# Optimization experiments

Measured on AMD Instinct MI355X. Metric: run time of the kernel, lower is better.

## Reference

```python
import jax, jax.numpy as jnp
import numpy as np

B, S, D, H, Dh, F = 1, 2048, 2048, 24, 128, 8192  # batch, seq, dim, heads, dim_head, ff hidden
SCALE = Dh ** -0.5


def _layernorm(x, g, b, eps=1e-5):
    mu = jnp.mean(x, axis=-1, keepdims=True)
    var = jnp.var(x, axis=-1, keepdims=True)
    return (x - mu) * jax.lax.rsqrt(var + eps) * g + b


def _rmsnorm(x, g, eps=1e-5):
    ms = jnp.mean(jnp.square(x), axis=-1, keepdims=True)
    return x * jax.lax.rsqrt(ms + eps) * g


def setup_inputs() -> dict:
    key = jax.random.key(0)
    ks = jax.random.split(key, 8)
    w = lambda k, sh: (jax.random.normal(k, sh, jnp.float32) * (1.0 / np.sqrt(sh[0]))).astype(jnp.float32)
    return {
        "x": jax.random.normal(ks[0], (B, S, D), jnp.float32),
        "ln_g": jnp.ones((D,), jnp.float32),
        "ln_b": jnp.zeros((D,), jnp.float32),
        "attn_g": jnp.ones((D,), jnp.float32),  # RingAttention prenorm (RMSNorm) gamma
        "Wq": w(ks[1], (D, H * Dh)),
        "Wk": w(ks[2], (D, H * Dh)),
        "Wv": w(ks[3], (D, H * Dh)),
        "Wo": w(ks[4], (H * Dh, D)),
        "W1": w(ks[5], (D, F)),
        "b1": jnp.zeros((F,), jnp.float32),
        "W2": w(ks[6], (F, D)),
        "b2": jnp.zeros((D,), jnp.float32),
    }


def reference(x, ln_g, ln_b, attn_g, Wq, Wk, Wv, Wo, W1, b1, W2, b2):
    # outer block LayerNorm
    x = _layernorm(x, ln_g, ln_b)

    # --- causal multi-head attention (math-equivalent to ring attention) ---
    h = _rmsnorm(x, attn_g)  # attention's internal prenorm
    q = (h @ Wq).reshape(B, S, H, Dh)
    k = (h @ Wk).reshape(B, S, H, Dh)
    v = (h @ Wv).reshape(B, S, H, Dh)
    scores = jnp.einsum("bqhd,bkhd->bhqk", q, k) * SCALE  # [B,H,S,S]
    causal = jnp.tril(jnp.ones((S, S), bool))
    scores = jnp.where(causal, scores, jnp.finfo(scores.dtype).min)
    attn = jax.nn.softmax(scores, axis=-1)
    o = jnp.einsum("bhqk,bkhd->bqhd", attn, v).reshape(B, S, H * Dh)
    x = o @ Wo + x  # residual

    # --- feedforward + residual ---
    x = jax.nn.gelu(x @ W1 + b1) @ W2 + b2 + x
    return x
```

## Files before the change

kernel.cpp:

```cpp
#include <hip/hip_runtime.h>
#include <hip/hip_bf16.h>

#define Sq 2048
#define Dm 2048
#define HDim 3072
#define QKVDim 9216
#define NH 24
#define DH 128
#define FF 8192
#define ATT_SCALE 0.08838834764831845f

using bf16 = __hip_bfloat16;
typedef __attribute__((ext_vector_type(8))) short bf16x8;
typedef __attribute__((ext_vector_type(4))) float f32x4;
typedef unsigned int u32;
typedef unsigned long long u64;
typedef __attribute__((ext_vector_type(4))) u32 u32x4;

__device__ __forceinline__ void gload_lds16(const void* g, void* l) {
    __builtin_amdgcn_global_load_lds(
        (const __attribute__((address_space(1))) void*)g,
        (__attribute__((address_space(3))) void*)l, 16, 0, 0);
}

__global__ __launch_bounds__(256) void ln_rms_kernel(
    const float* __restrict__ x, const float* __restrict__ g, const float* __restrict__ b,
    const float* __restrict__ ag, float* __restrict__ xnf, bf16* __restrict__ h)
{
    __shared__ float redA[4], redB[4], redC[4];
    int row = blockIdx.x;
    int t = threadIdx.x;
    int lane = t & 63, wid = t >> 6;
    const float* xr = x + (size_t)row * Dm;

    float v[8];
    float sum = 0.f, ssq = 0.f;
#pragma unroll
    for (int i = 0; i < 8; i++) {
        float f = xr[t + 256 * i];
        v[i] = f; sum += f; ssq += f * f;
    }
#pragma unroll
    for (int off = 32; off > 0; off >>= 1) {
        sum += __shfl_down(sum, off);
        ssq += __shfl_down(ssq, off);
    }
    if (lane == 0) { redA[wid] = sum; redB[wid] = ssq; }
    __syncthreads();
    sum = redA[0] + redA[1] + redA[2] + redA[3];
    ssq = redB[0] + redB[1] + redB[2] + redB[3];
    float mu = sum * (1.f / Dm);
    float var = ssq * (1.f / Dm) - mu * mu;
    float rstd = rsqrtf(var + 1e-5f);

    float xn[8];
    float s2 = 0.f;
#pragma unroll
    for (int i = 0; i < 8; i++) {
        int col = t + 256 * i;
        float xv = (v[i] - mu) * rstd * g[col] + b[col];
        xn[i] = xv;
        xnf[(size_t)row * Dm + col] = xv;
        s2 += xv * xv;
    }
#pragma unroll
    for (int off = 32; off > 0; off >>= 1) s2 += __shfl_down(s2, off);
    if (lane == 0) redC[wid] = s2;
    __syncthreads();
    s2 = redC[0] + redC[1] + redC[2] + redC[3];
    float rms = rsqrtf(s2 * (1.f / Dm) + 1e-5f);
#pragma unroll
    for (int i = 0; i < 8; i++) {
        int col = t + 256 * i;
        h[(size_t)row * Dm + col] = __float2bfloat16(xn[i] * rms * ag[col]);
    }
}

__global__ __launch_bounds__(256) void transpose_cvt_kernel(
    const float* __restrict__ W, bf16* __restrict__ Wt, int K, int N)
{
    __shared__ float tile[64][65];
    int n0 = blockIdx.x * 64, k0 = blockIdx.y * 64;
    int t = threadIdx.x;
    int lr = t >> 4, lc = (t & 15) * 4;
#pragma unroll
    for (int i = 0; i < 4; i++) {
        int r = lr + i * 16;
        f32x4 v = *reinterpret_cast<const f32x4*>(W + (size_t)(k0 + r) * N + n0 + lc);
        *reinterpret_cast<f32x4*>(&tile[r][lc]) = v;
    }
    __syncthreads();
    int nr = t >> 3, kc = (t & 7) * 8;
#pragma unroll
    for (int i = 0; i < 2; i++) {
        int n = nr + i * 32;
        bf16 o8[8];
#pragma unroll
        for (int j = 0; j < 8; j++) o8[j] = __float2bfloat16(tile[kc + j][n]);
        *reinterpret_cast<u32x4*>(Wt + (size_t)(n0 + n) * K + k0 + kc) =
            *reinterpret_cast<const u32x4*>(o8);
    }
}

__global__ __launch_bounds__(256) void transpose_cvt3_kernel(
    const float* __restrict__ Wa, const float* __restrict__ Wb, const float* __restrict__ Wc,
    bf16* __restrict__ Wt, int K, int N)
{
    __shared__ float tile[64][65];
    const float* W = blockIdx.z == 0 ? Wa : (blockIdx.z == 1 ? Wb : Wc);
    bf16* dst = Wt + (size_t)blockIdx.z * N * K;
    int n0 = blockIdx.x * 64, k0 = blockIdx.y * 64;
    int t = threadIdx.x;
    int lr = t >> 4, lc = (t & 15) * 4;
#pragma unroll
    for (int i = 0; i < 4; i++) {
        int r = lr + i * 16;
        f32x4 v = *reinterpret_cast<const f32x4*>(W + (size_t)(k0 + r) * N + n0 + lc);
        *reinterpret_cast<f32x4*>(&tile[r][lc]) = v;
    }
    __syncthreads();
    int nr = t >> 3, kc = (t & 7) * 8;
#pragma unroll
    for (int i = 0; i < 2; i++) {
        int n = nr + i * 32;
        bf16 o8[8];
#pragma unroll
        for (int j = 0; j < 8; j++) o8[j] = __float2bfloat16(tile[kc + j][n]);
        *reinterpret_cast<u32x4*>(dst + (size_t)(n0 + n) * K + k0 + kc) =
            *reinterpret_cast<const u32x4*>(o8);
    }
}

__global__ __launch_bounds__(256) void cvt_prefill_kernel(
    const float* __restrict__ xnf, const float* __restrict__ bias,
    bf16* __restrict__ hb, float* __restrict__ o, int N)
{
    int i = (blockIdx.x * 256 + threadIdx.x) * 8;
    int col = i % N;
    f32x4 a = *reinterpret_cast<const f32x4*>(xnf + i);
    f32x4 b = *reinterpret_cast<const f32x4*>(xnf + i + 4);
    bf16 r[8];
#pragma unroll
    for (int j = 0; j < 4; j++) { r[j] = __float2bfloat16(a[j]); r[4 + j] = __float2bfloat16(b[j]); }
    *reinterpret_cast<u32x4*>(hb + i) = *reinterpret_cast<const u32x4*>(r);
    f32x4 b0 = *reinterpret_cast<const f32x4*>(bias + col);
    f32x4 b1v = *reinterpret_cast<const f32x4*>(bias + col + 4);
    f32x4 o0 = {a[0] + b0[0], a[1] + b0[1], a[2] + b0[2], a[3] + b0[3]};
    f32x4 o1 = {b[0] + b1v[0], b[1] + b1v[1], b[2] + b1v[2], b[3] + b1v[3]};
    *reinterpret_cast<f32x4*>(o + i) = o0;
    *reinterpret_cast<f32x4*>(o + i + 4) = o1;
}

template <int EPI>
__global__ __launch_bounds__(256, 4) void gemm_kernel(
    const bf16* __restrict__ A, const bf16* __restrict__ Bt,
    int M, int N, int K, int Ksplit,
    bf16* Cb, float* Cf, const float* __restrict__ bias)
{
    __shared__ __align__(16) bf16 As[128 * 64];
    __shared__ __align__(16) bf16 Bs[128 * 64];
    int m0 = blockIdx.y * 128, n0 = blockIdx.x * 128;
    int kbeg = blockIdx.z * Ksplit, kend = kbeg + Ksplit;
    int tid = threadIdx.x;
    int lane = tid & 63, w = tid >> 6;
    int wr = w >> 1, wc = w & 1;
    int l15 = lane & 15, lhi = lane >> 4;

    int srow = lane >> 3;
    int scol = ((lane & 7) ^ (lane >> 3)) * 8;

    const f32x4 zero4 = {0.f, 0.f, 0.f, 0.f};
    f32x4 acc[4][4];
#pragma unroll
    for (int m = 0; m < 4; m++)
#pragma unroll
        for (int n = 0; n < 4; n++) acc[m][n] = zero4;

    for (int k0 = kbeg; k0 < kend; k0 += 64) {
        __syncthreads();
#pragma unroll
        for (int c = 0; c < 4; c++) {
            int row = w * 32 + c * 8 + srow;
            gload_lds16(A + (size_t)(m0 + row) * K + k0 + scol,
                        (char*)As + w * 4096 + c * 1024);
            gload_lds16(Bt + (size_t)(n0 + row) * K + k0 + scol,
                        (char*)Bs + w * 4096 + c * 1024);
        }
        __syncthreads();
#pragma unroll
        for (int ks = 0; ks < 2; ks++) {
            bf16x8 af[4], bfr[4];
#pragma unroll
            for (int m = 0; m < 4; m++) {
                int r = wr * 64 + m * 16 + l15;
                af[m] = *reinterpret_cast<const bf16x8*>(
                    &As[r * 64 + (((ks << 2) + lhi) ^ (r & 7)) * 8]);
            }
#pragma unroll
            for (int n = 0; n < 4; n++) {
                int r = wc * 64 + n * 16 + l15;
                bfr[n] = *reinterpret_cast<const bf16x8*>(
                    &Bs[r * 64 + (((ks << 2) + lhi) ^ (r & 7)) * 8]);
            }
#pragma unroll
            for (int m = 0; m < 4; m++)
#pragma unroll
                for (int n = 0; n < 4; n++)
                    acc[m][n] = __builtin_amdgcn_mfma_f32_16x16x32_bf16(af[m], bfr[n], acc[m][n], 0, 0, 0);
        }
    }

#pragma unroll
    for (int m = 0; m < 4; m++) {
        int row = m0 + wr * 64 + m * 16 + lhi * 4;
#pragma unroll
        for (int n = 0; n < 4; n++) {
            int col = n0 + wc * 64 + n * 16 + l15;
#pragma unroll
            for (int j = 0; j < 4; j++) {
                float vv = acc[m][n][j];
                size_t idx = (size_t)(row + j) * N + col;
                if (EPI == 0) {
                    Cb[idx] = __float2bfloat16(vv);
                } else if (EPI == 2) {
                    float o = vv + bias[col];
                    float u = 1.5957691216057308f * (o + 0.044715f * o * o * o);
                    Cb[idx] = __float2bfloat16(o / (1.0f + __expf(-u)));
                } else {
                    atomicAdd(&Cf[idx], vv);
                }
            }
        }
    }
}

__global__ __launch_bounds__(512) void attn_kernel(
    const bf16* __restrict__ qkv, bf16* __restrict__ o)
{
    __shared__ __align__(16) bf16 KsF[2][64 * 128];
    __shared__ __align__(16) bf16 VtF[128 * 72];
    __shared__ __align__(16) bf16 Pl[8][16][76];
    int rank = blockIdx.x;
    int qb = (Sq / 128 - 1) - rank / NH;
    int head = rank % NH;
    const bf16* q = qkv + head * DH;
    const bf16* k = qkv + HDim + head * DH;
    const bf16* v = qkv + 2 * HDim + head * DH;
    int tid = threadIdx.x, lane = tid & 63, w = tid >> 6;
    int l15 = lane & 15, lhi = lane >> 4;
    int qrow0 = qb * 128 + w * 16;

    bf16x8 aq[4];
    const bf16* qbase = q + (size_t)(qrow0 + l15) * QKVDim;
#pragma unroll
    for (int kk = 0; kk < 4; kk++)
        aq[kk] = *reinterpret_cast<const bf16x8*>(qbase + kk * 32 + lhi * 8);

    bf16x8 vones;
#pragma unroll
    for (int j = 0; j < 8; j++) vones[j] = (short)0x3F80;

    int vkv = lhi * 2 + (w & 1) + (w >> 1) * 8;
    int vd0 = l15 * 8;
    int vxr = l15 & 7;
    const bf16* vbase = v + (size_t)vkv * QKVDim + vd0;

    const f32x4 zero4 = {0.f, 0.f, 0.f, 0.f};
    f32x4 acc_o[8];
#pragma unroll
    for (int db = 0; db < 8; db++) acc_o[db] = zero4;
    f32x4 acc_l = zero4;
    float mrow[4];
#pragma unroll
    for (int r = 0; r < 4; r++) mrow[r] = -1e30f;

    int nt = 2 * qb + 2;

    {
#pragma unroll
        for (int c = 0; c < 2; c++) {
            int row = w * 8 + c * 4 + lhi;
            int cb = l15 ^ (row & 7);
            gload_lds16(k + (size_t)row * QKVDim + cb * 8,
                        (char*)&KsF[0][0] + w * 2048 + c * 1024);
        }
#pragma unroll
        for (int i = 0; i < 2; i++) {
            int kv = vkv + i * 32;
            bf16x8 vv = *reinterpret_cast<const bf16x8*>(vbase + (size_t)(i * 32) * QKVDim);
            int vb = kv >> 3, kr = kv & 7;
#pragma unroll
            for (int j = 0; j < 8; j++)
                VtF[(vd0 + j) * 72 + ((vb ^ vxr) << 3) + kr] = ((const bf16*)&vv)[j];
        }
        __syncthreads();
    }

    for (int kb = 0; kb < nt; kb++) {
        int kv0 = kb * 64;
        int p = kb & 1;
        bf16x8 vreg[2];
        bool pref = (kb + 1 < nt);
        if (pref) {
            int nv0 = kv0 + 64;
#pragma unroll
            for (int c = 0; c < 2; c++) {
                int row = w * 8 + c * 4 + lhi;
                int cb = l15 ^ (row & 7);
                gload_lds16(k + (size_t)(nv0 + row) * QKVDim + cb * 8,
                            (char*)&KsF[p ^ 1][0] + w * 2048 + c * 1024);
            }
#pragma unroll
            for (int i = 0; i < 2; i++)
                vreg[i] = *reinterpret_cast<const bf16x8*>(
                    vbase + (size_t)(nv0 + i * 32) * QKVDim);
        }

        bool active = (kv0 <= qrow0 + 15);
        if (active) {
            f32x4 sacc[4];
            __builtin_amdgcn_s_setprio(1);
#pragma unroll
            for (int nb = 0; nb < 4; nb++) {
                sacc[nb] = zero4;
                int krow = nb * 16 + l15;
#pragma unroll
                for (int kk = 0; kk < 4; kk++) {
                    const char* kp = (const char*)&KsF[p][0] + krow * 256 +
                                     ((kk * 64 + lhi * 16) ^ ((krow & 7) << 4));
                    bf16x8 bk = *reinterpret_cast<const bf16x8*>(kp);
                    sacc[nb] = __builtin_amdgcn_mfma_f32_16x16x32_bf16(aq[kk], bk, sacc[nb], 0, 0, 0);
                }
            }
            __builtin_amdgcn_s_setprio(0);

            bool msk = (kv0 + 63 > qrow0);
            float sv[4][4];
            float pm[4];
#pragma unroll
            for (int r = 0; r < 4; r++) pm[r] = -1e30f;
#pragma unroll
            for (int nb = 0; nb < 4; nb++) {
                int kvc = kv0 + nb * 16 + l15;
#pragma unroll
                for (int r = 0; r < 4; r++) {
                    int qr = qrow0 + lhi * 4 + r;
                    float s = sacc[nb][r] * ATT_SCALE;
                    if (msk && kvc > qr) s = -1e30f;
                    sv[nb][r] = s;
                    pm[r] = fmaxf(pm[r], s);
                }
            }
#pragma unroll
            for (int off = 1; off < 16; off <<= 1)
#pragma unroll
                for (int r = 0; r < 4; r++)
                    pm[r] = fmaxf(pm[r], __shfl_xor(pm[r], off));

            float nm[4];
            bool need = false;
#pragma unroll
            for (int r = 0; r < 4; r++) {
                nm[r] = fmaxf(mrow[r], pm[r]);
                need = need || (pm[r] > mrow[r] + 8.f);
            }
            if (__any(need)) {
#pragma unroll
                for (int r = 0; r < 4; r++) {
                    float sc = __expf(mrow[r] - nm[r]);
                    mrow[r] = nm[r];
                    acc_l[r] *= sc;
#pragma unroll
                    for (int db = 0; db < 8; db++) acc_o[db][r] *= sc;
                }
            }

#pragma unroll
            for (int nb = 0; nb < 4; nb++)
#pragma unroll
                for (int r = 0; r < 4; r++)
                    sv[nb][r] = __expf(sv[nb][r] - mrow[r]);

#pragma unroll
            for (int nb = 0; nb < 4; nb++)
#pragma unroll
                for (int r = 0; r < 4; r++)
                    Pl[w][lhi * 4 + r][nb * 16 + l15] = __float2bfloat16(sv[nb][r]);

            __builtin_amdgcn_s_setprio(1);
#pragma unroll
            for (int ks = 0; ks < 2; ks++) {
                bf16x8 ap = *reinterpret_cast<const bf16x8*>(&Pl[w][l15][ks * 32 + lhi * 8]);
                acc_l = __builtin_amdgcn_mfma_f32_16x16x32_bf16(ap, vones, acc_l, 0, 0, 0);
#pragma unroll
                for (int db = 0; db < 8; db++) {
                    int dv = db * 16 + l15;
                    int blk = (ks * 4 + lhi) ^ ((dv >> 3) & 7);
                    bf16x8 bv = *reinterpret_cast<const bf16x8*>(&VtF[dv * 72 + blk * 8]);
                    acc_o[db] = __builtin_amdgcn_mfma_f32_16x16x32_bf16(ap, bv, acc_o[db], 0, 0, 0);
                }
            }
            __builtin_amdgcn_s_setprio(0);
        }

        __syncthreads();
        if (pref) {
#pragma unroll
            for (int i = 0; i < 2; i++) {
                int kv = vkv + i * 32;
                int vb = kv >> 3, kr = kv & 7;
#pragma unroll
                for (int j = 0; j < 8; j++)
                    VtF[(vd0 + j) * 72 + ((vb ^ vxr) << 3) + kr] = ((const bf16*)&vreg[i])[j];
            }
        }
        __syncthreads();
    }

#pragma unroll
    for (int db = 0; db < 8; db++)
#pragma unroll
        for (int r = 0; r < 4; r++) {
            int qr = qrow0 + lhi * 4 + r;
            float val = acc_o[db][r] / acc_l[r];
            o[(size_t)qr * HDim + head * DH + db * 16 + l15] = __float2bfloat16(val);
        }
}

extern "C" void kernel_launch(void* const* d_in, const int* in_sizes, int n_in,
                              void* d_out, int out_size, void* d_ws, size_t ws_size,
                              hipStream_t stream)
{
    const float* x     = (const float*)d_in[0];
    const float* ln_g  = (const float*)d_in[1];
    const float* ln_b  = (const float*)d_in[2];
    const float* attng = (const float*)d_in[3];
    const float* Wq    = (const float*)d_in[4];
    const float* Wk    = (const float*)d_in[5];
    const float* Wv    = (const float*)d_in[6];
    const float* Wo    = (const float*)d_in[7];
    const float* W1    = (const float*)d_in[8];
    const float* b1    = (const float*)d_in[9];
    const float* W2    = (const float*)d_in[10];
    const float* b2    = (const float*)d_in[11];
    float* out = (float*)d_out;
    char* ws = (char*)d_ws;

    bf16*  wbuf = (bf16*)(ws + 0);
    float* xnf  = (float*)(ws + 39845888);
    bf16*  hbuf = (bf16*)(ws + 56623104);
    bf16*  qkv  = (bf16*)(ws + 65011712);
    bf16*  ob_  = (bf16*)(ws + 102760448);
    bf16*  gb_  = qkv;

    ln_rms_kernel<<<Sq, 256, 0, stream>>>(x, ln_g, ln_b, attng, xnf, hbuf);

    transpose_cvt3_kernel<<<dim3(HDim / 64, Dm / 64, 3), 256, 0, stream>>>(
        Wq, Wk, Wv, wbuf, Dm, HDim);
    gemm_kernel<0><<<dim3(QKVDim / 128, Sq / 128, 1), 256, 0, stream>>>(
        hbuf, wbuf, Sq, QKVDim, Dm, Dm, qkv, nullptr, nullptr);

    attn_kernel<<<dim3(NH * Sq / 128), 512, 0, stream>>>(qkv, ob_);

    transpose_cvt_kernel<<<dim3(Dm / 64, HDim / 64), 256, 0, stream>>>(Wo, wbuf, HDim, Dm);
    gemm_kernel<4><<<dim3(Dm / 128, Sq / 128, 2), 256, 0, stream>>>(
        ob_, wbuf, Sq, Dm, HDim, HDim / 2, nullptr, xnf, nullptr);
    cvt_prefill_kernel<<<(Sq * Dm) / (256 * 8), 256, 0, stream>>>(xnf, b2, hbuf, out, Dm);

    transpose_cvt_kernel<<<dim3(FF / 64, Dm / 64), 256, 0, stream>>>(W1, wbuf, Dm, FF);
    gemm_kernel<2><<<dim3(FF / 128, Sq / 128, 1), 256, 0, stream>>>(
        hbuf, wbuf, Sq, FF, Dm, Dm, gb_, nullptr, b1);

    transpose_cvt_kernel<<<dim3(Dm / 64, FF / 64), 256, 0, stream>>>(W2, wbuf, FF, Dm);
    gemm_kernel<4><<<dim3(Dm / 128, Sq / 128, 2), 256, 0, stream>>>(
        gb_, wbuf, Sq, Dm, FF, FF / 2, nullptr, out, nullptr);
}
```

Measured before the change: 449.3 us.

## Merge weight transposes into LN and attention launches; use exp2 softmax

The Wq/Wk/Wv transpose-convert now runs as extra blocks of the LayerNorm/RMSNorm kernel, and the Wo transpose as extra blocks of the attention kernel, each selected by block index and sharing LDS through a union. This removes two kernel launches and lets the independent transpose work fill idle compute units while the other blocks run. The attention softmax now folds log2(e) into the score scale and uses exp2f, with the rescale threshold adjusted to match. The cost is larger LDS and register footprints in the merged kernels, which may lower occupancy for the main work.

```diff
diff --git a/kernel.cpp b/kernel.cpp
--- a/kernel.cpp
+++ b/kernel.cpp
@@ -9,6 +9,7 @@
 #define DH 128
 #define FF 8192
 #define ATT_SCALE 0.08838834764831845f
+#define ATT_SCALE2 0.12752534331809017f
 
 using bf16 = __hip_bfloat16;
 typedef __attribute__((ext_vector_type(8))) short bf16x8;
@@ -23,13 +24,49 @@
         (__attribute__((address_space(3))) void*)l, 16, 0, 0);
 }
 
-__global__ __launch_bounds__(256) void ln_rms_kernel(
+__global__ __launch_bounds__(256) void ln_qkvt_kernel(
     const float* __restrict__ x, const float* __restrict__ g, const float* __restrict__ b,
-    const float* __restrict__ ag, float* __restrict__ xnf, bf16* __restrict__ h)
+    const float* __restrict__ ag, float* __restrict__ xnf, bf16* __restrict__ h,
+    const float* __restrict__ Wq, const float* __restrict__ Wk, const float* __restrict__ Wv,
+    bf16* __restrict__ Wt)
 {
-    __shared__ float redA[4], redB[4], redC[4];
-    int row = blockIdx.x;
+    union SmemU {
+        float red[12];
+        float tile[64][65];
+    };
+    __shared__ SmemU sm;
+    int bid = blockIdx.x;
     int t = threadIdx.x;
+
+    if (bid >= Sq) {
+        int tb = bid - Sq;
+        int z = tb / 1536, rr = tb % 1536;
+        int bx = rr % 48, by = rr / 48;
+        const float* W = z == 0 ? Wq : (z == 1 ? Wk : Wv);
+        bf16* dst = Wt + (size_t)z * HDim * Dm;
+        int n0 = bx * 64, k0 = by * 64;
+        int lr = t >> 4, lc = (t & 15) * 4;
+#pragma unroll
+        for (int i = 0; i < 4; i++) {
+            int r = lr + i * 16;
+            f32x4 v = *reinterpret_cast<const f32x4*>(W + (size_t)(k0 + r) * HDim + n0 + lc);
+            *reinterpret_cast<f32x4*>(&sm.tile[r][lc]) = v;
+        }
+        __syncthreads();
+        int nr = t >> 3, kc = (t & 7) * 8;
+#pragma unroll
+        for (int i = 0; i < 2; i++) {
+            int n = nr + i * 32;
+            bf16 o8[8];
+#pragma unroll
+            for (int j = 0; j < 8; j++) o8[j] = __float2bfloat16(sm.tile[kc + j][n]);
+            *reinterpret_cast<u32x4*>(dst + (size_t)(n0 + n) * Dm + k0 + kc) =
+                *reinterpret_cast<const u32x4*>(o8);
+        }
+        return;
+    }
+
+    int row = bid;
     int lane = t & 63, wid = t >> 6;
     const float* xr = x + (size_t)row * Dm;
 
@@ -45,10 +82,10 @@
         sum += __shfl_down(sum, off);
         ssq += __shfl_down(ssq, off);
     }
-    if (lane == 0) { redA[wid] = sum; redB[wid] = ssq; }
+    if (lane == 0) { sm.red[wid] = sum; sm.red[4 + wid] = ssq; }
     __syncthreads();
-    sum = redA[0] + redA[1] + redA[2] + redA[3];
-    ssq = redB[0] + redB[1] + redB[2] + redB[3];
+    sum = sm.red[0] + sm.red[1] + sm.red[2] + sm.red[3];
+    ssq = sm.red[4] + sm.red[5] + sm.red[6] + sm.red[7];
     float mu = sum * (1.f / Dm);
     float var = ssq * (1.f / Dm) - mu * mu;
     float rstd = rsqrtf(var + 1e-5f);
@@ -65,9 +102,9 @@
     }
 #pragma unroll
     for (int off = 32; off > 0; off >>= 1) s2 += __shfl_down(s2, off);
-    if (lane == 0) redC[wid] = s2;
+    if (lane == 0) sm.red[8 + wid] = s2;
     __syncthreads();
-    s2 = redC[0] + redC[1] + redC[2] + redC[3];
+    s2 = sm.red[8] + sm.red[9] + sm.red[10] + sm.red[11];
     float rms = rsqrtf(s2 * (1.f / Dm) + 1e-5f);
 #pragma unroll
     for (int i = 0; i < 8; i++) {
@@ -98,35 +135,6 @@
 #pragma unroll
         for (int j = 0; j < 8; j++) o8[j] = __float2bfloat16(tile[kc + j][n]);
         *reinterpret_cast<u32x4*>(Wt + (size_t)(n0 + n) * K + k0 + kc) =
-            *reinterpret_cast<const u32x4*>(o8);
-    }
-}
-
-__global__ __launch_bounds__(256) void transpose_cvt3_kernel(
-    const float* __restrict__ Wa, const float* __restrict__ Wb, const float* __restrict__ Wc,
-    bf16* __restrict__ Wt, int K, int N)
-{
-    __shared__ float tile[64][65];
-    const float* W = blockIdx.z == 0 ? Wa : (blockIdx.z == 1 ? Wb : Wc);
-    bf16* dst = Wt + (size_t)blockIdx.z * N * K;
-    int n0 = blockIdx.x * 64, k0 = blockIdx.y * 64;
-    int t = threadIdx.x;
-    int lr = t >> 4, lc = (t & 15) * 4;
-#pragma unroll
-    for (int i = 0; i < 4; i++) {
-        int r = lr + i * 16;
-        f32x4 v = *reinterpret_cast<const f32x4*>(W + (size_t)(k0 + r) * N + n0 + lc);
-        *reinterpret_cast<f32x4*>(&tile[r][lc]) = v;
-    }
-    __syncthreads();
-    int nr = t >> 3, kc = (t & 7) * 8;
-#pragma unroll
-    for (int i = 0; i < 2; i++) {
-        int n = nr + i * 32;
-        bf16 o8[8];
-#pragma unroll
-        for (int j = 0; j < 8; j++) o8[j] = __float2bfloat16(tile[kc + j][n]);
-        *reinterpret_cast<u32x4*>(dst + (size_t)(n0 + n) * K + k0 + kc) =
             *reinterpret_cast<const u32x4*>(o8);
     }
 }
@@ -235,18 +243,50 @@
 }
 
 __global__ __launch_bounds__(512) void attn_kernel(
-    const bf16* __restrict__ qkv, bf16* __restrict__ o)
+    const bf16* __restrict__ qkv, bf16* __restrict__ o,
+    const float* __restrict__ Wo, bf16* __restrict__ Wot)
 {
-    __shared__ __align__(16) bf16 KsF[2][64 * 128];
-    __shared__ __align__(16) bf16 VtF[128 * 72];
-    __shared__ __align__(16) bf16 Pl[8][16][76];
-    int rank = blockIdx.x;
+    struct AttnSmem {
+        bf16 KsF[2][64 * 128];
+        bf16 VtF[128 * 72];
+        bf16 Pl[8][16][76];
+    };
+    struct TransSmem { float tile[64][65]; };
+    union SmemU { AttnSmem a; TransSmem tp; };
+    __shared__ SmemU sm;
+
+    int bid = blockIdx.x;
+    int tid = threadIdx.x;
+    const int NATT = NH * (Sq / 128);
+
+    if (bid >= NATT) {
+        int tb = bid - NATT;
+        int bx = tb & 31, by = tb >> 5;
+        int n0 = bx * 64, k0 = by * 64;
+        int lr = tid >> 4, lc = (tid & 15) * 4;
+#pragma unroll
+        for (int i = 0; i < 2; i++) {
+            int r = lr + i * 32;
+            f32x4 v = *reinterpret_cast<const f32x4*>(Wo + (size_t)(k0 + r) * Dm + n0 + lc);
+            *reinterpret_cast<f32x4*>(&sm.tp.tile[r][lc]) = v;
+        }
+        __syncthreads();
+        int nr = tid >> 3, kc = (tid & 7) * 8;
+        bf16 o8[8];
+#pragma unroll
+        for (int j = 0; j < 8; j++) o8[j] = __float2bfloat16(sm.tp.tile[kc + j][nr]);
+        *reinterpret_cast<u32x4*>(Wot + (size_t)(n0 + nr) * HDim + k0 + kc) =
+            *reinterpret_cast<const u32x4*>(o8);
+        return;
+    }
+
+    int rank = bid;
     int qb = (Sq / 128 - 1) - rank / NH;
     int head = rank % NH;
     const bf16* q = qkv + head * DH;
     const bf16* k = qkv + HDim + head * DH;
     const bf16* v = qkv + 2 * HDim + head * DH;
-    int tid = threadIdx.x, lane = tid & 63, w = tid >> 6;
+    int lane = tid & 63, w = tid >> 6;
     int l15 = lane & 15, lhi = lane >> 4;
     int qrow0 = qb * 128 + w * 16;
 
@@ -282,7 +322,7 @@
             int row = w * 8 + c * 4 + lhi;
             int cb = l15 ^ (row & 7);
             gload_lds16(k + (size_t)row * QKVDim + cb * 8,
-                        (char*)&KsF[0][0] + w * 2048 + c * 1024);
+                        (char*)&sm.a.KsF[0][0] + w * 2048 + c * 1024);
         }
 #pragma unroll
         for (int i = 0; i < 2; i++) {
@@ -291,7 +331,7 @@
             int vb = kv >> 3, kr = kv & 7;
 #pragma unroll
             for (int j = 0; j < 8; j++)
-                VtF[(vd0 + j) * 72 + ((vb ^ vxr) << 3) + kr] = ((const bf16*)&vv)[j];
+                sm.a.VtF[(vd0 + j) * 72 + ((vb ^ vxr) << 3) + kr] = ((const bf16*)&vv)[j];
         }
         __syncthreads();
     }
@@ -308,7 +348,7 @@
                 int row = w * 8 + c * 4 + lhi;
                 int cb = l15 ^ (row & 7);
                 gload_lds16(k + (size_t)(nv0 + row) * QKVDim + cb * 8,
-                            (char*)&KsF[p ^ 1][0] + w * 2048 + c * 1024);
+                            (char*)&sm.a.KsF[p ^ 1][0] + w * 2048 + c * 1024);
             }
 #pragma unroll
             for (int i = 0; i < 2; i++)
@@ -326,7 +366,7 @@
                 int krow = nb * 16 + l15;
 #pragma unroll
                 for (int kk = 0; kk < 4; kk++) {
-                    const char* kp = (const char*)&KsF[p][0] + krow * 256 +
+                    const char* kp = (const char*)&sm.a.KsF[p][0] + krow * 256 +
                                      ((kk * 64 + lhi * 16) ^ ((krow & 7) << 4));
                     bf16x8 bk = *reinterpret_cast<const bf16x8*>(kp);
                     sacc[nb] = __builtin_amdgcn_mfma_f32_16x16x32_bf16(aq[kk], bk, sacc[nb], 0, 0, 0);
@@ -345,7 +385,7 @@
 #pragma unroll
                 for (int r = 0; r < 4; r++) {
                     int qr = qrow0 + lhi * 4 + r;
-                    float s = sacc[nb][r] * ATT_SCALE;
+                    float s = sacc[nb][r] * ATT_SCALE2;
                     if (msk && kvc > qr) s = -1e30f;
                     sv[nb][r] = s;
                     pm[r] = fmaxf(pm[r], s);
@@ -362,12 +402,12 @@
 #pragma unroll
             for (int r = 0; r < 4; r++) {
                 nm[r] = fmaxf(mrow[r], pm[r]);
-                need = need || (pm[r] > mrow[r] + 8.f);
+                need = need || (pm[r] > mrow[r] + 11.5f);
             }
             if (__any(need)) {
 #pragma unroll
                 for (int r = 0; r < 4; r++) {
-                    float sc = __expf(mrow[r] - nm[r]);
+                    float sc = exp2f(mrow[r] - nm[r]);
                     mrow[r] = nm[r];
                     acc_l[r] *= sc;
 #pragma unroll
@@ -379,24 +419,24 @@
             for (int nb = 0; nb < 4; nb++)
 #pragma unroll
                 for (int r = 0; r < 4; r++)
-                    sv[nb][r] = __expf(sv[nb][r] - mrow[r]);
+                    sv[nb][r] = exp2f(sv[nb][r] - mrow[r]);
 
 #pragma unroll
             for (int nb = 0; nb < 4; nb++)
 #pragma unroll
                 for (int r = 0; r < 4; r++)
-                    Pl[w][lhi * 4 + r][nb * 16 + l15] = __float2bfloat16(sv[nb][r]);
+                    sm.a.Pl[w][lhi * 4 + r][nb * 16 + l15] = __float2bfloat16(sv[nb][r]);
 
             __builtin_amdgcn_s_setprio(1);
 #pragma unroll
             for (int ks = 0; ks < 2; ks++) {
-                bf16x8 ap = *reinterpret_cast<const bf16x8*>(&Pl[w][l15][ks * 32 + lhi * 8]);
+                bf16x8 ap = *reinterpret_cast<const bf16x8*>(&sm.a.Pl[w][l15][ks * 32 + lhi * 8]);
                 acc_l = __builtin_amdgcn_mfma_f32_16x16x32_bf16(ap, vones, acc_l, 0, 0, 0);
 #pragma unroll
                 for (int db = 0; db < 8; db++) {
                     int dv = db * 16 + l15;
                     int blk = (ks * 4 + lhi) ^ ((dv >> 3) & 7);
-                    bf16x8 bv = *reinterpret_cast<const bf16x8*>(&VtF[dv * 72 + blk * 8]);
+                    bf16x8 bv = *reinterpret_cast<const bf16x8*>(&sm.a.VtF[dv * 72 + blk * 8]);
                     acc_o[db] = __builtin_amdgcn_mfma_f32_16x16x32_bf16(ap, bv, acc_o[db], 0, 0, 0);
                 }
             }
@@ -411,7 +451,7 @@
                 int vb = kv >> 3, kr = kv & 7;
 #pragma unroll
                 for (int j = 0; j < 8; j++)
-                    VtF[(vd0 + j) * 72 + ((vb ^ vxr) << 3) + kr] = ((const bf16*)&vreg[i])[j];
+                    sm.a.VtF[(vd0 + j) * 72 + ((vb ^ vxr) << 3) + kr] = ((const bf16*)&vreg[i])[j];
             }
         }
         __syncthreads();
@@ -453,16 +493,14 @@
     bf16*  ob_  = (bf16*)(ws + 102760448);
     bf16*  gb_  = qkv;
 
-    ln_rms_kernel<<<Sq, 256, 0, stream>>>(x, ln_g, ln_b, attng, xnf, hbuf);
-
-    transpose_cvt3_kernel<<<dim3(HDim / 64, Dm / 64, 3), 256, 0, stream>>>(
-        Wq, Wk, Wv, wbuf, Dm, HDim);
+    ln_qkvt_kernel<<<Sq + 3 * 1536, 256, 0, stream>>>(
+        x, ln_g, ln_b, attng, xnf, hbuf, Wq, Wk, Wv, wbuf);
+
     gemm_kernel<0><<<dim3(QKVDim / 128, Sq / 128, 1), 256, 0, stream>>>(
         hbuf, wbuf, Sq, QKVDim, Dm, Dm, qkv, nullptr, nullptr);
 
-    attn_kernel<<<dim3(NH * Sq / 128), 512, 0, stream>>>(qkv, ob_);
-
-    transpose_cvt_kernel<<<dim3(Dm / 64, HDim / 64), 256, 0, stream>>>(Wo, wbuf, HDim, Dm);
+    attn_kernel<<<dim3(NH * Sq / 128 + 1536), 512, 0, stream>>>(qkv, ob_, Wo, wbuf);
+
     gemm_kernel<4><<<dim3(Dm / 128, Sq / 128, 2), 256, 0, stream>>>(
         ob_, wbuf, Sq, Dm, HDim, HDim / 2, nullptr, xnf, nullptr);
     cvt_prefill_kernel<<<(Sq * Dm) / (256 * 8), 256, 0, stream>>>(xnf, b2, hbuf, out, Dm);
```

Result: slower. 481.1 us (+7.1%).
